# Kernel optimization log

Measured on AMD Instinct MI355X. Metric: run time of the kernel, lower is better.

## Reference

```python
import jax, jax.numpy as jnp
import numpy as np

N = 100000

def _gcn_layer(x, W, b, src, dst, norm):
    # dense transform then sparse normalized aggregation (scatter-add)
    h = x @ W                                  # [N, out]
    msg = h[src] * norm[:, None]               # [E+N, out]
    agg = jax.ops.segment_sum(msg, dst, num_segments=N)
    return agg + b


def setup_inputs() -> dict:
    key = jax.random.key(0)
    ks = jax.random.split(key, 12)
    num_features, hidden, num_classes = 128, 128, 32
    E = 3200000
    x = jax.random.normal(ks[0], (N, num_features), dtype=jnp.float32)
    edge_index = jax.random.randint(ks[1], (2, E), 0, N, dtype=jnp.int64)

    def glorot(k, fan_in, fan_out):
        s = (6.0 / (fan_in + fan_out)) ** 0.5
        return jax.random.uniform(k, (fan_in, fan_out), jnp.float32, -s, s)

    return {
        "x": x,
        "edge_index": edge_index,
        "W1": glorot(ks[2], num_features, hidden), "b1": jnp.zeros((hidden,), jnp.float32),
        "W2": glorot(ks[3], hidden, hidden),       "b2": jnp.zeros((hidden,), jnp.float32),
        "W3": glorot(ks[4], hidden, hidden),       "b3": jnp.zeros((hidden,), jnp.float32),
        "W4": glorot(ks[5], hidden, num_classes),  "b4": jnp.zeros((num_classes,), jnp.float32),
    }


def reference(x, edge_index, W1, b1, W2, b2, W3, b3, W4, b4):
    # GCNConv semantics: add self-loops, symmetric degree normalization
    loop = jnp.arange(N, dtype=edge_index.dtype)
    src = jnp.concatenate([edge_index[0], loop])   # [E+N]
    dst = jnp.concatenate([edge_index[1], loop])   # [E+N]
    deg = jax.ops.segment_sum(jnp.ones_like(dst, dtype=x.dtype), dst, num_segments=N)
    dinv = jnp.where(deg > 0, deg ** -0.5, 0.0)
    norm = dinv[src] * dinv[dst]                   # [E+N]

    h = _gcn_layer(x, W1, b1, src, dst, norm)
    h = jax.nn.relu(h)                              # dropout: eval mode -> identity
    h = _gcn_layer(h, W2, b2, src, dst, norm)
    h = jax.nn.relu(h)
    h = _gcn_layer(h, W3, b3, src, dst, norm)
    h = jax.nn.relu(h)
    h = _gcn_layer(h, W4, b4, src, dst, norm)
    return jax.nn.log_softmax(h, axis=1)
```

## Files before the change

### kernel.cpp

```cpp
#include <hip/hip_runtime.h>
#include <hip/hip_bf16.h>
#include <math.h>

#define NNODES 100000
#define NBMAX 512
#define CH 8192

typedef __hip_bfloat16 bf16;
typedef __attribute__((ext_vector_type(8))) short short8;
typedef __attribute__((ext_vector_type(4))) float f32x4;
typedef __attribute__((ext_vector_type(2))) float f32x2;

__device__ inline unsigned pack_bf16x2(float a, float b) {
    __hip_bfloat162 p;
    p.x = __float2bfloat16(a);
    p.y = __float2bfloat16(b);
    return *(unsigned*)&p;
}

__device__ inline float2 unpack_bf16x2(unsigned u) {
    __hip_bfloat162 p = *(__hip_bfloat162*)&u;
    return make_float2(__bfloat162float(p.x), __bfloat162float(p.y));
}

__device__ inline unsigned char f32_to_fp8(float v) {
    int p = __builtin_amdgcn_cvt_pk_fp8_f32(v, v, 0, false);
    return (unsigned char)(p & 0xff);
}

__global__ __launch_bounds__(256) void bucket_hist(const int* __restrict__ dst,
                                                   int* __restrict__ bcount, int E, int nb) {
    __shared__ int hist[NBMAX];
    int t = threadIdx.x;
    for (int i = t; i < NBMAX; i += 256) hist[i] = 0;
    __syncthreads();
    int e0 = blockIdx.x * CH;
#pragma unroll
    for (int k = 0; k < 32; ++k) {
        int e = e0 + t + k * 256;
        if (e < E) atomicAdd(&hist[dst[e] >> 8], 1);
    }
    __syncthreads();
    for (int i = t; i < nb; i += 256)
        if (hist[i]) atomicAdd(&bcount[i], hist[i]);
}

__global__ __launch_bounds__(512) void bucket_scan(const int* __restrict__ bcount,
                                                   int* __restrict__ boff,
                                                   int* __restrict__ bcursor,
                                                   int* __restrict__ off, int nb, int n) {
    __shared__ int wsum[8];
    int t = threadIdx.x;
    int v = (t < nb) ? bcount[t] : 0;
    int lane = t & 63, wv = t >> 6;
    int incl = v;
#pragma unroll
    for (int d = 1; d < 64; d <<= 1) {
        int x = __shfl_up(incl, d, 64);
        if (lane >= d) incl += x;
    }
    if (lane == 63) wsum[wv] = incl;
    __syncthreads();
    int wo = 0;
    for (int k = 0; k < wv; ++k) wo += wsum[k];
    int excl = wo + incl - v;
    if (t <= nb) {
        boff[t] = excl;
        if (t < nb) bcursor[t] = excl;
    }
    if (t == nb) off[n] = excl;
}

__global__ __launch_bounds__(256) void partition(const int* __restrict__ src,
                                                 const int* __restrict__ dst,
                                                 int* __restrict__ bcursor,
                                                 int2* __restrict__ part, int E, int nb) {
    __shared__ int hist[NBMAX];
    __shared__ int lstart[NBMAX];
    __shared__ int gbase[NBMAX];
    __shared__ int cursor[NBMAX];
    __shared__ int2 sorted[CH];
    int t = threadIdx.x;
    int e0 = blockIdx.x * CH;
    for (int i = t; i < NBMAX; i += 256) hist[i] = 0;
    __syncthreads();
    int mys[32], myd[32];
#pragma unroll
    for (int k = 0; k < 32; ++k) {
        int e = e0 + t + k * 256;
        int s = 0, d = -1;
        if (e < E) { s = src[e]; d = dst[e]; }
        mys[k] = s; myd[k] = d;
        if (d >= 0) atomicAdd(&hist[d >> 8], 1);
    }
    __syncthreads();
    if (t < 64) {
        int base = t * 8;
        int tmp[8];
        int sum = 0;
#pragma unroll
        for (int j = 0; j < 8; ++j) { tmp[j] = hist[base + j]; sum += tmp[j]; }
        int incl = sum;
#pragma unroll
        for (int d = 1; d < 64; d <<= 1) {
            int x = __shfl_up(incl, d, 64);
            if (t >= d) incl += x;
        }
        int excl = incl - sum;
#pragma unroll
        for (int j = 0; j < 8; ++j) {
            lstart[base + j] = excl;
            cursor[base + j] = excl;
            excl += tmp[j];
        }
    }
    __syncthreads();
    for (int i = t; i < nb; i += 256) {
        int c = hist[i];
        gbase[i] = c ? atomicAdd(&bcursor[i], c) : 0;
    }
    __syncthreads();
#pragma unroll
    for (int k = 0; k < 32; ++k) {
        int d = myd[k];
        if (d >= 0) {
            int lpos = atomicAdd(&cursor[d >> 8], 1);
            sorted[lpos] = make_int2(mys[k], d);
        }
    }
    __syncthreads();
    int cnt = min(CH, E - e0);
    for (int i = t; i < cnt; i += 256) {
        int2 rec = sorted[i];
        int b = rec.y >> 8;
        part[gbase[b] + (i - lstart[b])] = rec;
    }
}

__global__ __launch_bounds__(256) void bucket_nodes(const int2* __restrict__ part,
                                                    const int* __restrict__ boff,
                                                    float* __restrict__ dinv,
                                                    int* __restrict__ off, int n) {
    __shared__ int ndeg[256];
    __shared__ int ws2[4];
    int b = blockIdx.x;
    int t = threadIdx.x;
    ndeg[t] = 0;
    __syncthreads();
    int r0 = boff[b], r1 = boff[b + 1];
    for (int i = r0 + t; i < r1; i += 256)
        atomicAdd(&ndeg[part[i].y & 255], 1);
    __syncthreads();
    int deg = ndeg[t];
    int node = b * 256 + t;
    int lane = t & 63, wv = t >> 6;
    int incl = deg;
#pragma unroll
    for (int d = 1; d < 64; d <<= 1) {
        int x = __shfl_up(incl, d, 64);
        if (lane >= d) incl += x;
    }
    if (lane == 63) ws2[wv] = incl;
    __syncthreads();
    int wo = 0;
    for (int k = 0; k < wv; ++k) wo += ws2[k];
    if (node < n) {
        off[node] = r0 + wo + incl - deg;
        dinv[node] = rsqrtf((float)(deg + 1));
    }
}

__global__ __launch_bounds__(256) void fine_fill(const int2* __restrict__ part,
                                                 const int* __restrict__ boff,
                                                 const int* __restrict__ off,
                                                 int* __restrict__ edges, int n) {
    __shared__ int cur[256];
    __shared__ int offl[256];
    int b = blockIdx.x;
    int t = threadIdx.x;
    int node = b * 256 + t;
    cur[t] = 0;
    offl[t] = (node < n) ? off[node] : 0;
    __syncthreads();
    int r0 = boff[b], r1 = boff[b + 1];
    for (int i = r0 + t; i < r1; i += 256) {
        int2 rec = part[i];
        int dloc = rec.y & 255;
        int lpos = atomicAdd(&cur[dloc], 1);
        edges[offl[dloc] + lpos] = rec.x;
    }
}

__global__ void prep_w(const float* __restrict__ W, bf16* __restrict__ WT, int K, int Nout) {
    int idx = blockIdx.x * blockDim.x + threadIdx.x;
    if (idx >= K * Nout) return;
    int nn = idx / K;
    int kk = idx - nn * K;
    WT[idx] = __float2bfloat16(W[kk * Nout + nn]);
}

#define WSTRIDE 136

__global__ __launch_bounds__(256) void gemm128_f32A(const float* __restrict__ A,
                                                    const bf16* __restrict__ WT,
                                                    const float* __restrict__ dinv,
                                                    unsigned char* __restrict__ C, int n) {
    __shared__ bf16 wl[128 * WSTRIDE];
    int t = threadIdx.x;
#pragma unroll
    for (int l = 0; l < 8; ++l) {
        int chunk = t + l * 256;
        int row = chunk >> 4, ch = chunk & 15;
        *(uint4*)&wl[row * WSTRIDE + ch * 8] = *(const uint4*)&WT[row * 128 + ch * 8];
    }
    __syncthreads();
    int wave = t >> 6, lane = t & 63;
    int m = lane & 15, q = lane >> 4;
    int row_base = blockIdx.x * 128 + wave * 32;
    int r0 = min(row_base + m, n - 1);
    int r1 = min(row_base + 16 + m, n - 1);

    f32x4 acc[2][8];
#pragma unroll
    for (int g = 0; g < 2; ++g)
#pragma unroll
        for (int c = 0; c < 8; ++c) acc[g][c] = (f32x4)(0.f);

#pragma unroll
    for (int kt = 0; kt < 4; ++kt) {
        short8 af[2];
#pragma unroll
        for (int g = 0; g < 2; ++g) {
            const float* ap = &A[(size_t)(g ? r1 : r0) * 128 + kt * 32 + q * 8];
            float4 f0 = *(const float4*)ap;
            float4 f1 = *(const float4*)(ap + 4);
            union { uint4 u; short8 s; } cv;
            cv.u.x = pack_bf16x2(f0.x, f0.y);
            cv.u.y = pack_bf16x2(f0.z, f0.w);
            cv.u.z = pack_bf16x2(f1.x, f1.y);
            cv.u.w = pack_bf16x2(f1.z, f1.w);
            af[g] = cv.s;
        }
#pragma unroll
        for (int c = 0; c < 8; ++c) {
            short8 bf = *(const short8*)&wl[(c * 16 + m) * WSTRIDE + kt * 32 + q * 8];
            acc[0][c] = __builtin_amdgcn_mfma_f32_16x16x32_bf16(af[0], bf, acc[0][c], 0, 0, 0);
            acc[1][c] = __builtin_amdgcn_mfma_f32_16x16x32_bf16(af[1], bf, acc[1][c], 0, 0, 0);
        }
    }
    float dv[2][4];
#pragma unroll
    for (int g = 0; g < 2; ++g)
#pragma unroll
        for (int r = 0; r < 4; ++r) {
            int row = row_base + g * 16 + q * 4 + r;
            dv[g][r] = (row < n) ? dinv[row] : 0.f;
        }
#pragma unroll
    for (int g = 0; g < 2; ++g)
#pragma unroll
        for (int c = 0; c < 8; ++c)
#pragma unroll
            for (int r = 0; r < 4; ++r) {
                int row = row_base + g * 16 + q * 4 + r;
                if (row < n) C[(size_t)row * 128 + c * 16 + m] = f32_to_fp8(acc[g][c][r] * dv[g][r]);
            }
}

__global__ __launch_bounds__(256) void gemm128_bf16A(const bf16* __restrict__ A,
                                                     const bf16* __restrict__ WT,
                                                     const float* __restrict__ dinv,
                                                     unsigned char* __restrict__ C, int n) {
    __shared__ bf16 wl[128 * WSTRIDE];
    int t = threadIdx.x;
#pragma unroll
    for (int l = 0; l < 8; ++l) {
        int chunk = t + l * 256;
        int row = chunk >> 4, ch = chunk & 15;
        *(uint4*)&wl[row * WSTRIDE + ch * 8] = *(const uint4*)&WT[row * 128 + ch * 8];
    }
    __syncthreads();
    int wave = t >> 6, lane = t & 63;
    int m = lane & 15, q = lane >> 4;
    int row_base = blockIdx.x * 128 + wave * 32;
    int r0 = min(row_base + m, n - 1);
    int r1 = min(row_base + 16 + m, n - 1);

    f32x4 acc[2][8];
#pragma unroll
    for (int g = 0; g < 2; ++g)
#pragma unroll
        for (int c = 0; c < 8; ++c) acc[g][c] = (f32x4)(0.f);

#pragma unroll
    for (int kt = 0; kt < 4; ++kt) {
        short8 a0 = *(const short8*)&A[(size_t)r0 * 128 + kt * 32 + q * 8];
        short8 a1 = *(const short8*)&A[(size_t)r1 * 128 + kt * 32 + q * 8];
#pragma unroll
        for (int c = 0; c < 8; ++c) {
            short8 bf = *(const short8*)&wl[(c * 16 + m) * WSTRIDE + kt * 32 + q * 8];
            acc[0][c] = __builtin_amdgcn_mfma_f32_16x16x32_bf16(a0, bf, acc[0][c], 0, 0, 0);
            acc[1][c] = __builtin_amdgcn_mfma_f32_16x16x32_bf16(a1, bf, acc[1][c], 0, 0, 0);
        }
    }
    float dv[2][4];
#pragma unroll
    for (int g = 0; g < 2; ++g)
#pragma unroll
        for (int r = 0; r < 4; ++r) {
            int row = row_base + g * 16 + q * 4 + r;
            dv[g][r] = (row < n) ? dinv[row] : 0.f;
        }
#pragma unroll
    for (int g = 0; g < 2; ++g)
#pragma unroll
        for (int c = 0; c < 8; ++c)
#pragma unroll
            for (int r = 0; r < 4; ++r) {
                int row = row_base + g * 16 + q * 4 + r;
                if (row < n) C[(size_t)row * 128 + c * 16 + m] = f32_to_fp8(acc[g][c][r] * dv[g][r]);
            }
}

__global__ __launch_bounds__(256) void gemm32_bf16A(const bf16* __restrict__ A,
                                                    const bf16* __restrict__ WT,
                                                    const float* __restrict__ dinv,
                                                    bf16* __restrict__ C, int n) {
    int wave = threadIdx.x >> 6;
    int lane = threadIdx.x & 63;
    int m = lane & 15;
    int q = lane >> 4;
    int row_base = blockIdx.x * 64 + wave * 16;
    int arow = min(row_base + m, n - 1);

    f32x4 acc[2];
    acc[0] = (f32x4)(0.f);
    acc[1] = (f32x4)(0.f);

#pragma unroll
    for (int kt = 0; kt < 4; ++kt) {
        short8 af = *(const short8*)&A[(size_t)arow * 128 + kt * 32 + q * 8];
#pragma unroll
        for (int c = 0; c < 2; ++c) {
            short8 bf = *(const short8*)&WT[(size_t)(c * 16 + m) * 128 + kt * 32 + q * 8];
            acc[c] = __builtin_amdgcn_mfma_f32_16x16x32_bf16(af, bf, acc[c], 0, 0, 0);
        }
    }
    float dv[4];
#pragma unroll
    for (int r = 0; r < 4; ++r) {
        int row = row_base + q * 4 + r;
        dv[r] = (row < n) ? dinv[row] : 0.f;
    }
#pragma unroll
    for (int c = 0; c < 2; ++c)
#pragma unroll
        for (int r = 0; r < 4; ++r) {
            int row = row_base + q * 4 + r;
            if (row < n) C[(size_t)row * 32 + c * 16 + m] = __float2bfloat16(acc[c][r] * dv[r]);
        }
}

__global__ __launch_bounds__(256) void agg128(const unsigned char* __restrict__ h,
                                              const int* __restrict__ off,
                                              const int* __restrict__ edges,
                                              const float* __restrict__ dinv,
                                              const float* __restrict__ bias,
                                              bf16* __restrict__ out, int n) {
    int wid = (blockIdx.x * blockDim.x + threadIdx.x) >> 6;
    if (wid >= n) return;
    int lane = threadIdx.x & 63;
    int half = lane >> 5;
    int pos = lane & 31;
    const unsigned* h32 = (const unsigned*)h;

    unsigned su = half ? 0u : h32[(size_t)wid * 32 + pos];
    f32x2 accL = __builtin_amdgcn_cvt_pk_f32_fp8((int)su, false);
    f32x2 accH = __builtin_amdgcn_cvt_pk_f32_fp8((int)su, true);

    int i0 = off[wid], i1 = off[wid + 1];
    int i = i0;
    for (; i + 32 <= i1; i += 32) {
        unsigned uu[16];
#pragma unroll
        for (int j = 0; j < 16; ++j) {
            int s = edges[i + j * 2 + half];
            uu[j] = h32[(size_t)s * 32 + pos];
        }
#pragma unroll
        for (int j = 0; j < 16; ++j) {
            accL += __builtin_amdgcn_cvt_pk_f32_fp8((int)uu[j], false);
            accH += __builtin_amdgcn_cvt_pk_f32_fp8((int)uu[j], true);
        }
    }
    for (; i + 8 <= i1; i += 8) {
        unsigned uu[4];
#pragma unroll
        for (int j = 0; j < 4; ++j) {
            int s = edges[i + j * 2 + half];
            uu[j] = h32[(size_t)s * 32 + pos];
        }
#pragma unroll
        for (int j = 0; j < 4; ++j) {
            accL += __builtin_amdgcn_cvt_pk_f32_fp8((int)uu[j], false);
            accH += __builtin_amdgcn_cvt_pk_f32_fp8((int)uu[j], true);
        }
    }
    for (; i + 2 <= i1; i += 2) {
        int s = edges[i + half];
        unsigned u = h32[(size_t)s * 32 + pos];
        accL += __builtin_amdgcn_cvt_pk_f32_fp8((int)u, false);
        accH += __builtin_amdgcn_cvt_pk_f32_fp8((int)u, true);
    }
    if (i < i1) {
        unsigned u = half ? 0u : h32[(size_t)edges[i] * 32 + pos];
        accL += __builtin_amdgcn_cvt_pk_f32_fp8((int)u, false);
        accH += __builtin_amdgcn_cvt_pk_f32_fp8((int)u, true);
    }
    float a0 = accL[0] + __shfl_xor(accL[0], 32);
    float a1 = accL[1] + __shfl_xor(accL[1], 32);
    float a2 = accH[0] + __shfl_xor(accH[0], 32);
    float a3 = accH[1] + __shfl_xor(accH[1], 32);

    float dl = dinv[wid];
    float4 bv = ((const float4*)bias)[pos];
    a0 = fmaxf(a0 * dl + bv.x, 0.f);
    a1 = fmaxf(a1 * dl + bv.y, 0.f);
    a2 = fmaxf(a2 * dl + bv.z, 0.f);
    a3 = fmaxf(a3 * dl + bv.w, 0.f);
    unsigned pk = half ? pack_bf16x2(a2, a3) : pack_bf16x2(a0, a1);
    ((unsigned*)out)[(size_t)wid * 64 + pos * 2 + half] = pk;
}

__global__ __launch_bounds__(256) void agg32_lsm(const bf16* __restrict__ h,
                                                 const int* __restrict__ off,
                                                 const int* __restrict__ edges,
                                                 const float* __restrict__ dinv,
                                                 const float* __restrict__ bias,
                                                 float* __restrict__ out, int n) {
    int idx = blockIdx.x * blockDim.x + threadIdx.x;
    int node = idx >> 5;
    if (node >= n) return;
    int lane5 = idx & 31;
    int sub = lane5 & 15;
    int pr = lane5 >> 4;
    const unsigned* h4 = (const unsigned*)h;

    unsigned su = pr ? 0u : h4[(size_t)node * 16 + sub];
    float2 sf = unpack_bf16x2(su);
    f32x2 acc = {sf.x, sf.y};

    int i0 = off[node], i1 = off[node + 1];
    int i = i0;
    for (; i + 16 <= i1; i += 16) {
        unsigned uu[8];
#pragma unroll
        for (int j = 0; j < 8; ++j) {
            int s = edges[i + j * 2 + pr];
            uu[j] = h4[(size_t)s * 16 + sub];
        }
#pragma unroll
        for (int j = 0; j < 8; ++j) {
            float2 f = unpack_bf16x2(uu[j]);
            acc[0] += f.x; acc[1] += f.y;
        }
    }
    for (; i + 2 <= i1; i += 2) {
        int s = edges[i + pr];
        float2 f = unpack_bf16x2(h4[(size_t)s * 16 + sub]);
        acc[0] += f.x; acc[1] += f.y;
    }
    if (i < i1) {
        unsigned u = pr ? 0u : h4[(size_t)edges[i] * 16 + sub];
        float2 f = unpack_bf16x2(u);
        acc[0] += f.x; acc[1] += f.y;
    }
    float s0 = acc[0] + __shfl_xor(acc[0], 16);
    float s1 = acc[1] + __shfl_xor(acc[1], 16);

    float dl = dinv[node];
    float2 bv = *(const float2*)&bias[sub * 2];
    float a0 = s0 * dl + bv.x;
    float a1 = s1 * dl + bv.y;
    float m = fmaxf(a0, a1);
    for (int d = 8; d; d >>= 1) m = fmaxf(m, __shfl_xor(m, d));
    float e = expf(a0 - m) + expf(a1 - m);
    for (int d = 8; d; d >>= 1) e += __shfl_xor(e, d);
    float lse = m + logf(e);
    if (pr == 0)
        *(float2*)&out[(size_t)node * 32 + sub * 2] = make_float2(a0 - lse, a1 - lse);
}

extern "C" void kernel_launch(void* const* d_in, const int* in_sizes, int n_in,
                              void* d_out, int out_size, void* d_ws, size_t ws_size,
                              hipStream_t stream) {
    const float* x  = (const float*)d_in[0];
    const int*   ei = (const int*)d_in[1];
    const float* W1 = (const float*)d_in[2];
    const float* b1 = (const float*)d_in[3];
    const float* W2 = (const float*)d_in[4];
    const float* b2 = (const float*)d_in[5];
    const float* W3 = (const float*)d_in[6];
    const float* b3 = (const float*)d_in[7];
    const float* W4 = (const float*)d_in[8];
    const float* b4 = (const float*)d_in[9];
    float* out = (float*)d_out;

    const int N = NNODES;
    const int E = in_sizes[1] / 2;
    const int nb = (N + 255) / 256;

    char* ws = (char*)d_ws;
    size_t o = 0;
    auto alloc = [&](size_t bytes) -> void* {
        void* p = ws + o;
        o += (bytes + 255) & ~(size_t)255;
        return p;
    };
    int*   bcount  = (int*)alloc((size_t)NBMAX * 4);
    int*   boff    = (int*)alloc((size_t)(NBMAX + 1) * 4);
    int*   bcursor = (int*)alloc((size_t)NBMAX * 4);
    int*   off     = (int*)alloc((size_t)(N + 1) * 4);
    float* dinv    = (float*)alloc((size_t)N * 4);
    int2*  part    = (int2*)alloc((size_t)E * 8);
    int*   edges   = (int*)alloc((size_t)E * 4);
    bf16*  wt1     = (bf16*)alloc((size_t)128 * 128 * 2);
    bf16*  wt2     = (bf16*)alloc((size_t)128 * 128 * 2);
    bf16*  wt3     = (bf16*)alloc((size_t)128 * 128 * 2);
    bf16*  wt4     = (bf16*)alloc((size_t)32 * 128 * 2);
    unsigned char* hbuf = (unsigned char*)alloc((size_t)N * 128);
    bf16*  gbuf    = (bf16*)part;

    const int* srcv = ei;
    const int* dstv = ei + E;

    hipMemsetAsync(bcount, 0, (size_t)NBMAX * 4, stream);

    int pblocks = (E + CH - 1) / CH;
    bucket_hist<<<pblocks, 256, 0, stream>>>(dstv, bcount, E, nb);
    bucket_scan<<<1, 512, 0, stream>>>(bcount, boff, bcursor, off, nb, N);
    partition<<<pblocks, 256, 0, stream>>>(srcv, dstv, bcursor, part, E, nb);
    bucket_nodes<<<nb, 256, 0, stream>>>(part, boff, dinv, off, N);
    fine_fill<<<nb, 256, 0, stream>>>(part, boff, off, edges, N);

    prep_w<<<64, 256, 0, stream>>>(W1, wt1, 128, 128);
    prep_w<<<64, 256, 0, stream>>>(W2, wt2, 128, 128);
    prep_w<<<64, 256, 0, stream>>>(W3, wt3, 128, 128);
    prep_w<<<16, 256, 0, stream>>>(W4, wt4, 128, 32);

    int gemm128_blocks = (N + 127) / 128;
    int gemm32_blocks = (N + 63) / 64;
    int agg128_blocks = (N + 3) / 4;
    int agg32_blocks = (N * 32 + 255) / 256;

    gemm128_f32A<<<gemm128_blocks, 256, 0, stream>>>(x, wt1, dinv, hbuf, N);
    agg128<<<agg128_blocks, 256, 0, stream>>>(hbuf, off, edges, dinv, b1, gbuf, N);
    gemm128_bf16A<<<gemm128_blocks, 256, 0, stream>>>(gbuf, wt2, dinv, hbuf, N);
    agg128<<<agg128_blocks, 256, 0, stream>>>(hbuf, off, edges, dinv, b2, gbuf, N);
    gemm128_bf16A<<<gemm128_blocks, 256, 0, stream>>>(gbuf, wt3, dinv, hbuf, N);
    agg128<<<agg128_blocks, 256, 0, stream>>>(hbuf, off, edges, dinv, b3, gbuf, N);
    gemm32_bf16A<<<gemm32_blocks, 256, 0, stream>>>(gbuf, wt4, dinv, (bf16*)hbuf, N);
    agg32_lsm<<<agg32_blocks, 256, 0, stream>>>((const bf16*)hbuf, off, edges, dinv, b4, out, N);
}
```

Measured before the change: 517.2 us.

## Split fp8 features into 64-byte planes and pack partition records into 32 bits

The GEMM epilogues now write the fp8 hidden features as two feature planes of 64 bytes per node instead of 128-byte rows. agg128 walks each plane in turn, with four edges in flight per wave (16 lanes per edge), so every gather touches a 64-byte segment and fewer bytes per cache line go unused. The partition records are packed into one 32-bit word (17-bit source, 8-bit local destination), halving the traffic of the partition, bucket_nodes and fine_fill passes. agg32_lsm moves to one wave per node with four edge lanes. The two-pass walk rereads the edge list for every node, and the packing assumes node ids fit in 17 bits.

```diff
diff --git a/kernel.cpp b/kernel.cpp
--- a/kernel.cpp
+++ b/kernel.cpp
@@ -74,7 +74,7 @@
 __global__ __launch_bounds__(256) void partition(const int* __restrict__ src,
                                                  const int* __restrict__ dst,
                                                  int* __restrict__ bcursor,
-                                                 int2* __restrict__ part, int E, int nb) {
+                                                 unsigned* __restrict__ part, int E, int nb) {
     __shared__ int hist[NBMAX];
     __shared__ int lstart[NBMAX];
     __shared__ int gbase[NBMAX];
@@ -133,11 +133,12 @@
     for (int i = t; i < cnt; i += 256) {
         int2 rec = sorted[i];
         int b = rec.y >> 8;
-        part[gbase[b] + (i - lstart[b])] = rec;
-    }
-}
-
-__global__ __launch_bounds__(256) void bucket_nodes(const int2* __restrict__ part,
+        unsigned pk = ((unsigned)(rec.y & 255) << 17) | (unsigned)rec.x;
+        part[gbase[b] + (i - lstart[b])] = pk;
+    }
+}
+
+__global__ __launch_bounds__(256) void bucket_nodes(const unsigned* __restrict__ part,
                                                     const int* __restrict__ boff,
                                                     float* __restrict__ dinv,
                                                     int* __restrict__ off, int n) {
@@ -149,7 +150,7 @@
     __syncthreads();
     int r0 = boff[b], r1 = boff[b + 1];
     for (int i = r0 + t; i < r1; i += 256)
-        atomicAdd(&ndeg[part[i].y & 255], 1);
+        atomicAdd(&ndeg[part[i] >> 17], 1);
     __syncthreads();
     int deg = ndeg[t];
     int node = b * 256 + t;
@@ -170,7 +171,7 @@
     }
 }
 
-__global__ __launch_bounds__(256) void fine_fill(const int2* __restrict__ part,
+__global__ __launch_bounds__(256) void fine_fill(const unsigned* __restrict__ part,
                                                  const int* __restrict__ boff,
                                                  const int* __restrict__ off,
                                                  int* __restrict__ edges, int n) {
@@ -184,10 +185,10 @@
     __syncthreads();
     int r0 = boff[b], r1 = boff[b + 1];
     for (int i = r0 + t; i < r1; i += 256) {
-        int2 rec = part[i];
-        int dloc = rec.y & 255;
+        unsigned rec = part[i];
+        int dloc = rec >> 17;
         int lpos = atomicAdd(&cur[dloc], 1);
-        edges[offl[dloc] + lpos] = rec.x;
+        edges[offl[dloc] + lpos] = (int)(rec & 0x1FFFFu);
     }
 }
 
@@ -256,15 +257,19 @@
             int row = row_base + g * 16 + q * 4 + r;
             dv[g][r] = (row < n) ? dinv[row] : 0.f;
         }
+    size_t plane = (size_t)n * 64;
 #pragma unroll
     for (int g = 0; g < 2; ++g)
 #pragma unroll
-        for (int c = 0; c < 8; ++c)
+        for (int c = 0; c < 8; ++c) {
+            int f = c * 16 + m;
+            size_t base = (size_t)(f >> 6) * plane + (f & 63);
 #pragma unroll
             for (int r = 0; r < 4; ++r) {
                 int row = row_base + g * 16 + q * 4 + r;
-                if (row < n) C[(size_t)row * 128 + c * 16 + m] = f32_to_fp8(acc[g][c][r] * dv[g][r]);
+                if (row < n) C[base + (size_t)row * 64] = f32_to_fp8(acc[g][c][r] * dv[g][r]);
             }
+        }
 }
 
 __global__ __launch_bounds__(256) void gemm128_bf16A(const bf16* __restrict__ A,
@@ -311,15 +316,19 @@
             int row = row_base + g * 16 + q * 4 + r;
             dv[g][r] = (row < n) ? dinv[row] : 0.f;
         }
+    size_t plane = (size_t)n * 64;
 #pragma unroll
     for (int g = 0; g < 2; ++g)
 #pragma unroll
-        for (int c = 0; c < 8; ++c)
+        for (int c = 0; c < 8; ++c) {
+            int f = c * 16 + m;
+            size_t base = (size_t)(f >> 6) * plane + (f & 63);
 #pragma unroll
             for (int r = 0; r < 4; ++r) {
                 int row = row_base + g * 16 + q * 4 + r;
-                if (row < n) C[(size_t)row * 128 + c * 16 + m] = f32_to_fp8(acc[g][c][r] * dv[g][r]);
+                if (row < n) C[base + (size_t)row * 64] = f32_to_fp8(acc[g][c][r] * dv[g][r]);
             }
+        }
 }
 
 __global__ __launch_bounds__(256) void gemm32_bf16A(const bf16* __restrict__ A,
@@ -370,66 +379,72 @@
     int wid = (blockIdx.x * blockDim.x + threadIdx.x) >> 6;
     if (wid >= n) return;
     int lane = threadIdx.x & 63;
-    int half = lane >> 5;
-    int pos = lane & 31;
-    const unsigned* h32 = (const unsigned*)h;
-
-    unsigned su = half ? 0u : h32[(size_t)wid * 32 + pos];
-    f32x2 accL = __builtin_amdgcn_cvt_pk_f32_fp8((int)su, false);
-    f32x2 accH = __builtin_amdgcn_cvt_pk_f32_fp8((int)su, true);
-
+    int sub = lane & 15;
+    int pr = lane >> 4;
     int i0 = off[wid], i1 = off[wid + 1];
-    int i = i0;
-    for (; i + 32 <= i1; i += 32) {
-        unsigned uu[16];
-#pragma unroll
-        for (int j = 0; j < 16; ++j) {
-            int s = edges[i + j * 2 + half];
-            uu[j] = h32[(size_t)s * 32 + pos];
-        }
-#pragma unroll
-        for (int j = 0; j < 16; ++j) {
-            accL += __builtin_amdgcn_cvt_pk_f32_fp8((int)uu[j], false);
-            accH += __builtin_amdgcn_cvt_pk_f32_fp8((int)uu[j], true);
-        }
-    }
-    for (; i + 8 <= i1; i += 8) {
-        unsigned uu[4];
-#pragma unroll
-        for (int j = 0; j < 4; ++j) {
-            int s = edges[i + j * 2 + half];
-            uu[j] = h32[(size_t)s * 32 + pos];
-        }
-#pragma unroll
-        for (int j = 0; j < 4; ++j) {
-            accL += __builtin_amdgcn_cvt_pk_f32_fp8((int)uu[j], false);
-            accH += __builtin_amdgcn_cvt_pk_f32_fp8((int)uu[j], true);
-        }
-    }
-    for (; i + 2 <= i1; i += 2) {
-        int s = edges[i + half];
-        unsigned u = h32[(size_t)s * 32 + pos];
-        accL += __builtin_amdgcn_cvt_pk_f32_fp8((int)u, false);
-        accH += __builtin_amdgcn_cvt_pk_f32_fp8((int)u, true);
-    }
-    if (i < i1) {
-        unsigned u = half ? 0u : h32[(size_t)edges[i] * 32 + pos];
-        accL += __builtin_amdgcn_cvt_pk_f32_fp8((int)u, false);
-        accH += __builtin_amdgcn_cvt_pk_f32_fp8((int)u, true);
-    }
-    float a0 = accL[0] + __shfl_xor(accL[0], 32);
-    float a1 = accL[1] + __shfl_xor(accL[1], 32);
-    float a2 = accH[0] + __shfl_xor(accH[0], 32);
-    float a3 = accH[1] + __shfl_xor(accH[1], 32);
-
     float dl = dinv[wid];
-    float4 bv = ((const float4*)bias)[pos];
-    a0 = fmaxf(a0 * dl + bv.x, 0.f);
-    a1 = fmaxf(a1 * dl + bv.y, 0.f);
-    a2 = fmaxf(a2 * dl + bv.z, 0.f);
-    a3 = fmaxf(a3 * dl + bv.w, 0.f);
-    unsigned pk = half ? pack_bf16x2(a2, a3) : pack_bf16x2(a0, a1);
-    ((unsigned*)out)[(size_t)wid * 64 + pos * 2 + half] = pk;
+    unsigned* outp = (unsigned*)out + (size_t)wid * 64;
+
+#pragma unroll
+    for (int p = 0; p < 2; ++p) {
+        const unsigned* hp = (const unsigned*)(h + (size_t)p * n * 64);
+        unsigned su = (pr == 0) ? hp[(size_t)wid * 16 + sub] : 0u;
+        f32x2 accL = __builtin_amdgcn_cvt_pk_f32_fp8((int)su, false);
+        f32x2 accH = __builtin_amdgcn_cvt_pk_f32_fp8((int)su, true);
+        int i = i0;
+        for (; i + 64 <= i1; i += 64) {
+            unsigned uu[16];
+#pragma unroll
+            for (int j = 0; j < 16; ++j) {
+                int s = edges[i + j * 4 + pr];
+                uu[j] = hp[(size_t)s * 16 + sub];
+            }
+#pragma unroll
+            for (int j = 0; j < 16; ++j) {
+                accL += __builtin_amdgcn_cvt_pk_f32_fp8((int)uu[j], false);
+                accH += __builtin_amdgcn_cvt_pk_f32_fp8((int)uu[j], true);
+            }
+        }
+        for (; i + 16 <= i1; i += 16) {
+            unsigned uu[4];
+#pragma unroll
+            for (int j = 0; j < 4; ++j) {
+                int s = edges[i + j * 4 + pr];
+                uu[j] = hp[(size_t)s * 16 + sub];
+            }
+#pragma unroll
+            for (int j = 0; j < 4; ++j) {
+                accL += __builtin_amdgcn_cvt_pk_f32_fp8((int)uu[j], false);
+                accH += __builtin_amdgcn_cvt_pk_f32_fp8((int)uu[j], true);
+            }
+        }
+        for (; i + 4 <= i1; i += 4) {
+            int s = edges[i + pr];
+            unsigned u = hp[(size_t)s * 16 + sub];
+            accL += __builtin_amdgcn_cvt_pk_f32_fp8((int)u, false);
+            accH += __builtin_amdgcn_cvt_pk_f32_fp8((int)u, true);
+        }
+        if (i < i1) {
+            int rem = i1 - i;
+            unsigned u = (pr < rem) ? hp[(size_t)edges[i + pr] * 16 + sub] : 0u;
+            accL += __builtin_amdgcn_cvt_pk_f32_fp8((int)u, false);
+            accH += __builtin_amdgcn_cvt_pk_f32_fp8((int)u, true);
+        }
+        float a0 = accL[0], a1 = accL[1], a2 = accH[0], a3 = accH[1];
+        a0 += __shfl_xor(a0, 16); a0 += __shfl_xor(a0, 32);
+        a1 += __shfl_xor(a1, 16); a1 += __shfl_xor(a1, 32);
+        a2 += __shfl_xor(a2, 16); a2 += __shfl_xor(a2, 32);
+        a3 += __shfl_xor(a3, 16); a3 += __shfl_xor(a3, 32);
+        if (pr == 0) {
+            float4 bv = ((const float4*)bias)[p * 16 + sub];
+            a0 = fmaxf(a0 * dl + bv.x, 0.f);
+            a1 = fmaxf(a1 * dl + bv.y, 0.f);
+            a2 = fmaxf(a2 * dl + bv.z, 0.f);
+            a3 = fmaxf(a3 * dl + bv.w, 0.f);
+            uint2 pk = make_uint2(pack_bf16x2(a0, a1), pack_bf16x2(a2, a3));
+            *(uint2*)&outp[p * 32 + sub * 2] = pk;
+        }
+    }
 }
 
 __global__ __launch_bounds__(256) void agg32_lsm(const bf16* __restrict__ h,
@@ -438,57 +453,57 @@
                                                  const float* __restrict__ dinv,
                                                  const float* __restrict__ bias,
                                                  float* __restrict__ out, int n) {
-    int idx = blockIdx.x * blockDim.x + threadIdx.x;
-    int node = idx >> 5;
-    if (node >= n) return;
-    int lane5 = idx & 31;
-    int sub = lane5 & 15;
-    int pr = lane5 >> 4;
+    int wid = (blockIdx.x * blockDim.x + threadIdx.x) >> 6;
+    if (wid >= n) return;
+    int lane = threadIdx.x & 63;
+    int sub = lane & 15;
+    int pr = lane >> 4;
     const unsigned* h4 = (const unsigned*)h;
 
-    unsigned su = pr ? 0u : h4[(size_t)node * 16 + sub];
+    unsigned su = (pr == 0) ? h4[(size_t)wid * 16 + sub] : 0u;
     float2 sf = unpack_bf16x2(su);
-    f32x2 acc = {sf.x, sf.y};
-
-    int i0 = off[node], i1 = off[node + 1];
+    float acc0 = sf.x, acc1 = sf.y;
+
+    int i0 = off[wid], i1 = off[wid + 1];
     int i = i0;
-    for (; i + 16 <= i1; i += 16) {
+    for (; i + 32 <= i1; i += 32) {
         unsigned uu[8];
 #pragma unroll
         for (int j = 0; j < 8; ++j) {
-            int s = edges[i + j * 2 + pr];
+            int s = edges[i + j * 4 + pr];
             uu[j] = h4[(size_t)s * 16 + sub];
         }
 #pragma unroll
         for (int j = 0; j < 8; ++j) {
             float2 f = unpack_bf16x2(uu[j]);
-            acc[0] += f.x; acc[1] += f.y;
-        }
-    }
-    for (; i + 2 <= i1; i += 2) {
+            acc0 += f.x; acc1 += f.y;
+        }
+    }
+    for (; i + 4 <= i1; i += 4) {
         int s = edges[i + pr];
         float2 f = unpack_bf16x2(h4[(size_t)s * 16 + sub]);
-        acc[0] += f.x; acc[1] += f.y;
+        acc0 += f.x; acc1 += f.y;
     }
     if (i < i1) {
-        unsigned u = pr ? 0u : h4[(size_t)edges[i] * 16 + sub];
+        int rem = i1 - i;
+        unsigned u = (pr < rem) ? h4[(size_t)edges[i + pr] * 16 + sub] : 0u;
         float2 f = unpack_bf16x2(u);
-        acc[0] += f.x; acc[1] += f.y;
-    }
-    float s0 = acc[0] + __shfl_xor(acc[0], 16);
-    float s1 = acc[1] + __shfl_xor(acc[1], 16);
-
-    float dl = dinv[node];
+        acc0 += f.x; acc1 += f.y;
+    }
+    acc0 += __shfl_xor(acc0, 16); acc0 += __shfl_xor(acc0, 32);
+    acc1 += __shfl_xor(acc1, 16); acc1 += __shfl_xor(acc1, 32);
+
+    float dl = dinv[wid];
     float2 bv = *(const float2*)&bias[sub * 2];
-    float a0 = s0 * dl + bv.x;
-    float a1 = s1 * dl + bv.y;
+    float a0 = acc0 * dl + bv.x;
+    float a1 = acc1 * dl + bv.y;
     float m = fmaxf(a0, a1);
     for (int d = 8; d; d >>= 1) m = fmaxf(m, __shfl_xor(m, d));
     float e = expf(a0 - m) + expf(a1 - m);
     for (int d = 8; d; d >>= 1) e += __shfl_xor(e, d);
     float lse = m + logf(e);
     if (pr == 0)
-        *(float2*)&out[(size_t)node * 32 + sub * 2] = make_float2(a0 - lse, a1 - lse);
+        *(float2*)&out[(size_t)wid * 32 + sub * 2] = make_float2(a0 - lse, a1 - lse);
 }
 
 extern "C" void kernel_launch(void* const* d_in, const int* in_sizes, int n_in,
@@ -517,19 +532,19 @@
         o += (bytes + 255) & ~(size_t)255;
         return p;
     };
-    int*   bcount  = (int*)alloc((size_t)NBMAX * 4);
-    int*   boff    = (int*)alloc((size_t)(NBMAX + 1) * 4);
-    int*   bcursor = (int*)alloc((size_t)NBMAX * 4);
-    int*   off     = (int*)alloc((size_t)(N + 1) * 4);
-    float* dinv    = (float*)alloc((size_t)N * 4);
-    int2*  part    = (int2*)alloc((size_t)E * 8);
-    int*   edges   = (int*)alloc((size_t)E * 4);
-    bf16*  wt1     = (bf16*)alloc((size_t)128 * 128 * 2);
-    bf16*  wt2     = (bf16*)alloc((size_t)128 * 128 * 2);
-    bf16*  wt3     = (bf16*)alloc((size_t)128 * 128 * 2);
-    bf16*  wt4     = (bf16*)alloc((size_t)32 * 128 * 2);
+    int*      bcount  = (int*)alloc((size_t)NBMAX * 4);
+    int*      boff    = (int*)alloc((size_t)(NBMAX + 1) * 4);
+    int*      bcursor = (int*)alloc((size_t)NBMAX * 4);
+    int*      off     = (int*)alloc((size_t)(N + 1) * 4);
+    float*    dinv    = (float*)alloc((size_t)N * 4);
+    unsigned* part    = (unsigned*)alloc((size_t)E * 8);
+    int*      edges   = (int*)alloc((size_t)E * 4);
+    bf16*     wt1     = (bf16*)alloc((size_t)128 * 128 * 2);
+    bf16*     wt2     = (bf16*)alloc((size_t)128 * 128 * 2);
+    bf16*     wt3     = (bf16*)alloc((size_t)128 * 128 * 2);
+    bf16*     wt4     = (bf16*)alloc((size_t)32 * 128 * 2);
     unsigned char* hbuf = (unsigned char*)alloc((size_t)N * 128);
-    bf16*  gbuf    = (bf16*)part;
+    bf16*     gbuf    = (bf16*)part;
 
     const int* srcv = ei;
     const int* dstv = ei + E;
@@ -550,15 +565,14 @@
 
     int gemm128_blocks = (N + 127) / 128;
     int gemm32_blocks = (N + 63) / 64;
-    int agg128_blocks = (N + 3) / 4;
-    int agg32_blocks = (N * 32 + 255) / 256;
+    int wave_blocks = (N + 3) / 4;
 
     gemm128_f32A<<<gemm128_blocks, 256, 0, stream>>>(x, wt1, dinv, hbuf, N);
-    agg128<<<agg128_blocks, 256, 0, stream>>>(hbuf, off, edges, dinv, b1, gbuf, N);
+    agg128<<<wave_blocks, 256, 0, stream>>>(hbuf, off, edges, dinv, b1, gbuf, N);
     gemm128_bf16A<<<gemm128_blocks, 256, 0, stream>>>(gbuf, wt2, dinv, hbuf, N);
-    agg128<<<agg128_blocks, 256, 0, stream>>>(hbuf, off, edges, dinv, b2, gbuf, N);
+    agg128<<<wave_blocks, 256, 0, stream>>>(hbuf, off, edges, dinv, b2, gbuf, N);
     gemm128_bf16A<<<gemm128_blocks, 256, 0, stream>>>(gbuf, wt3, dinv, hbuf, N);
-    agg128<<<agg128_blocks, 256, 0, stream>>>(hbuf, off, edges, dinv, b3, gbuf, N);
+    agg128<<<wave_blocks, 256, 0, stream>>>(hbuf, off, edges, dinv, b3, gbuf, N);
     gemm32_bf16A<<<gemm32_blocks, 256, 0, stream>>>(gbuf, wt4, dinv, (bf16*)hbuf, N);
-    agg32_lsm<<<agg32_blocks, 256, 0, stream>>>((const bf16*)hbuf, off, edges, dinv, b4, out, N);
-}
+    agg32_lsm<<<wave_blocks, 256, 0, stream>>>((const bf16*)hbuf, off, edges, dinv, b4, out, N);
+}
```

Measured after the change: 807.8 us. +56.2%, slower.
